# Kernel tuning notes

Measured on AMD Instinct MI355X. Metric: run time of the kernel, lower is better.

## Reference

```python
import jax, jax.numpy as jnp
import numpy as np

N = 16384          # num nodes (128 graphs x 128 turbines)
E = 262144         # edges before self loops
TURBINE_NUM = 128
D_IN = 512         # input_dim (= 2*hidden_dim1)
H1 = 256           # hidden_dim1
H2 = 256           # hidden_dim2
NEG_SLOPE = 0.2    # PyG GATConv default leaky relu slope


def _glorot(key, shape, fan_in):
    return jax.random.normal(key, shape, dtype=jnp.float32) / np.sqrt(fan_in)


def setup_inputs() -> dict:
    key = jax.random.key(0)
    ks = jax.random.split(key, 12)
    x = jax.random.normal(ks[0], (N, H2), dtype=jnp.float32)
    adj = jax.random.randint(ks[1], (2, E), 0, N, dtype=jnp.int64)
    # fc: Linear(hidden_dim2 -> hidden_dim1); stored as [in, out]
    W_fc = _glorot(ks[2], (H2, H1), H2)
    b_fc = jnp.zeros((H1,), dtype=jnp.float32)
    # gat1: GATConv(H1 -> H1, heads=2, concat)
    W1 = _glorot(ks[3], (H1, 2 * H1), H1)
    a1_src = _glorot(ks[4], (2, H1), H1)
    a1_dst = _glorot(ks[5], (2, H1), H1)
    b1 = jnp.zeros((2 * H1,), dtype=jnp.float32)
    # gat2: GATConv(D_IN -> D_IN, heads=1, concat)
    W2 = _glorot(ks[6], (D_IN, D_IN), D_IN)
    a2_src = _glorot(ks[7], (1, D_IN), D_IN)
    a2_dst = _glorot(ks[8], (1, D_IN), D_IN)
    b2 = jnp.zeros((D_IN,), dtype=jnp.float32)
    return dict(x=x, adj=adj, W_fc=W_fc, b_fc=b_fc, W1=W1, a1_src=a1_src,
                a1_dst=a1_dst, b1=b1, W2=W2, a2_src=a2_src, a2_dst=a2_dst, b2=b2)


def gat_conv(x, src, dst, W, a_src, a_dst, bias, heads, out_ch):
    """PyG GATConv (eval mode, self loops already in src/dst)."""
    n = x.shape[0]
    h = (x @ W).reshape(n, heads, out_ch)                 # [N,H,C]
    al_s = jnp.einsum('nhc,hc->nh', h, a_src)             # [N,H]
    al_d = jnp.einsum('nhc,hc->nh', h, a_dst)
    e = jax.nn.leaky_relu(al_s[src] + al_d[dst], NEG_SLOPE)  # [E,H]
    # segment softmax over incoming edges per destination node
    e_max = jax.ops.segment_max(e, dst, num_segments=n)
    e_exp = jnp.exp(e - e_max[dst])
    denom = jax.ops.segment_sum(e_exp, dst, num_segments=n)
    alpha = e_exp / (denom[dst] + 1e-16)                  # [E,H]
    msg = h[src] * alpha[:, :, None]                      # [E,H,C]
    out = jax.ops.segment_sum(msg, dst, num_segments=n)   # [N,H,C]
    return out.reshape(n, heads * out_ch) + bias


def reference(x, adj, W_fc, b_fc, W1, a1_src, a1_dst, b1, W2, a2_src, a2_dst, b2):
    # add self loops (PyG GATConv default)
    loops = jnp.arange(N, dtype=adj.dtype)
    src = jnp.concatenate([adj[0], loops])
    dst = jnp.concatenate([adj[1], loops])
    h = jax.nn.relu(x @ W_fc + b_fc)                      # fc + ReLU
    h = gat_conv(h, src, dst, W1, a1_src, a1_dst, b1, heads=2, out_ch=H1)
    h = jax.nn.relu(h)
    h = gat_conv(h, src, dst, W2, a2_src, a2_dst, b2, heads=1, out_ch=D_IN)
    y = jax.nn.relu(h)
    return y.reshape(-1, TURBINE_NUM, y.shape[1])         # [128,128,512]
```

## Files before the change

kernel.cpp:

```cpp
#include <hip/hip_runtime.h>

#define N_NODES 16384
#define N_EDGES 262144
#define E_TOT   (N_EDGES + N_NODES)
#define NEG_SLOPE 0.2f

typedef __attribute__((ext_vector_type(8))) short short8;
typedef __attribute__((ext_vector_type(4))) float floatx4;
typedef __attribute__((ext_vector_type(4))) int intx4;

__device__ __forceinline__ float bf2f(ushort u) {
    return __uint_as_float(((unsigned)u) << 16);
}
__device__ __forceinline__ ushort f2bf(float f) {
    unsigned u = __float_as_uint(f);
    u += 0x7fffu + ((u >> 16) & 1u);
    return (ushort)(u >> 16);
}
__device__ __forceinline__ float leaky(float x) {
    return x > 0.f ? x : NEG_SLOPE * x;
}

#define PREP_CAST   524288
#define PREP_T0     (PREP_CAST)
#define PREP_T1     (PREP_T0 + 65536)
#define PREP_T2     (PREP_T1 + 131072)
#define PREP_Z      (PREP_T2 + 262144)
#define PREP_ZA     (PREP_Z + 4096)
#define PREP_TOT    (PREP_ZA + 24576)

__global__ __launch_bounds__(256) void k_prep(const float* __restrict__ x,
                                              ushort* __restrict__ xb,
                                              const float* __restrict__ Wfc,
                                              ushort* __restrict__ WfcT,
                                              const float* __restrict__ W1,
                                              ushort* __restrict__ W1T,
                                              const float* __restrict__ W2,
                                              ushort* __restrict__ W2T,
                                              int* __restrict__ counts,
                                              int* __restrict__ alzero) {
    int idx = blockIdx.x * 256 + threadIdx.x;
    if (idx < PREP_CAST) {
        floatx4 v0 = *(const floatx4*)(x + (size_t)idx * 8);
        floatx4 v1 = *(const floatx4*)(x + (size_t)idx * 8 + 4);
        short8 r;
        r[0] = (short)f2bf(v0[0]); r[1] = (short)f2bf(v0[1]);
        r[2] = (short)f2bf(v0[2]); r[3] = (short)f2bf(v0[3]);
        r[4] = (short)f2bf(v1[0]); r[5] = (short)f2bf(v1[1]);
        r[6] = (short)f2bf(v1[2]); r[7] = (short)f2bf(v1[3]);
        *(short8*)(xb + (size_t)idx * 8) = r;
    } else if (idx < PREP_T1) {
        int t = idx - PREP_T0;
        int k = t >> 8, n = t & 255;
        WfcT[n * 256 + k] = f2bf(Wfc[t]);
    } else if (idx < PREP_T2) {
        int t = idx - PREP_T1;
        int k = t >> 9, n = t & 511;
        W1T[n * 256 + k] = f2bf(W1[t]);
    } else if (idx < PREP_Z) {
        int t = idx - PREP_T2;
        int k = t >> 9, n = t & 511;
        W2T[n * 512 + k] = f2bf(W2[t]);
    } else if (idx < PREP_ZA) {
        int t = idx - PREP_Z;
        *(intx4*)(counts + t * 4) = (intx4){0, 0, 0, 0};
    } else if (idx < PREP_TOT) {
        int t = idx - PREP_ZA;
        *(intx4*)(alzero + t * 4) = (intx4){0, 0, 0, 0};
    }
}

__global__ __launch_bounds__(256) void k_hist(const int* __restrict__ adj,
                                              int* __restrict__ counts) {
    int e = blockIdx.x * 256 + threadIdx.x;
    if (e < E_TOT) {
        int d = (e < N_EDGES) ? adj[N_EDGES + e] : (e - N_EDGES);
        atomicAdd(&counts[d], 1);
    }
}

__global__ __launch_bounds__(1024) void k_scan(const int* __restrict__ counts,
                                               int* __restrict__ offs,
                                               int* __restrict__ cursor) {
    __shared__ int wsum[16];
    int t = threadIdx.x, lane = t & 63, w = t >> 6;
    int local[16];
    int tot = 0;
#pragma unroll
    for (int i = 0; i < 16; i++) {
        local[i] = tot;
        tot += counts[t * 16 + i];
    }
    int incl = tot;
#pragma unroll
    for (int d = 1; d < 64; d <<= 1) {
        int v = __shfl_up(incl, d, 64);
        if (lane >= d) incl += v;
    }
    if (lane == 63) wsum[w] = incl;
    __syncthreads();
    if (w == 0) {
        int v = (lane < 16) ? wsum[lane] : 0;
#pragma unroll
        for (int d = 1; d < 16; d <<= 1) {
            int u = __shfl_up(v, d, 64);
            if (lane >= d) v += u;
        }
        if (lane < 16) wsum[lane] = v;
    }
    __syncthreads();
    int base = ((w == 0) ? 0 : wsum[w - 1]) + incl - tot;
#pragma unroll
    for (int i = 0; i < 16; i++) {
        int o = base + local[i];
        offs[t * 16 + i] = o;
        cursor[t * 16 + i] = o;
    }
    if (t == 1023) offs[N_NODES] = wsum[15];
}

__global__ __launch_bounds__(256) void k_scatter(const int* __restrict__ adj,
                                                 int* __restrict__ cursor,
                                                 int* __restrict__ esrc) {
    int e = blockIdx.x * 256 + threadIdx.x;
    if (e < E_TOT) {
        int s, d;
        if (e < N_EDGES) { s = adj[e]; d = adj[N_EDGES + e]; }
        else             { s = e - N_EDGES; d = s; }
        int pos = atomicAdd(&cursor[d], 1);
        esrc[pos] = s;
    }
}

#define GM 128
#define GN 128
#define GK 64
#define LDK2 72

__global__ __launch_bounds__(256) void gemm128(const ushort* __restrict__ A,
                                               const ushort* __restrict__ BT,
                                               const float* __restrict__ bias,
                                               ushort* __restrict__ C,
                                               int M, int Nc, int K, int relu,
                                               const float* __restrict__ asrc,
                                               const float* __restrict__ adst,
                                               float* __restrict__ als,
                                               float* __restrict__ ald,
                                               int heads) {
    __shared__ ushort As[GM * LDK2];
    __shared__ ushort Bs[GN * LDK2];
    int tid = threadIdx.x, wave = tid >> 6, lane = tid & 63;
    int quad = lane >> 4, l16 = lane & 15;
    int bm = blockIdx.x * GM, bn = blockIdx.y * GN;
    int wm = (wave & 1) * 64, wn = (wave >> 1) * 64;

    floatx4 acc[4][4];
#pragma unroll
    for (int mi = 0; mi < 4; mi++)
#pragma unroll
        for (int ni = 0; ni < 4; ni++)
            acc[mi][ni] = (floatx4){0.f, 0.f, 0.f, 0.f};

    for (int kb = 0; kb < K; kb += GK) {
        short8 av[4], bv[4];
#pragma unroll
        for (int t = 0; t < 4; t++) {
            int ci = tid + 256 * t;
            int row = ci >> 3, col = (ci & 7) * 8;
            av[t] = *(const short8*)(A + (size_t)(bm + row) * K + kb + col);
            bv[t] = *(const short8*)(BT + (size_t)(bn + row) * K + kb + col);
        }
        __syncthreads();
#pragma unroll
        for (int t = 0; t < 4; t++) {
            int ci = tid + 256 * t;
            int row = ci >> 3, col = (ci & 7) * 8;
            *(short8*)&As[row * LDK2 + col] = av[t];
            *(short8*)&Bs[row * LDK2 + col] = bv[t];
        }
        __syncthreads();

#pragma unroll
        for (int kk = 0; kk < GK; kk += 32) {
            short8 af[4], bf[4];
#pragma unroll
            for (int mi = 0; mi < 4; mi++)
                af[mi] = *(const short8*)&As[(wm + mi * 16 + l16) * LDK2 + kk + quad * 8];
#pragma unroll
            for (int ni = 0; ni < 4; ni++)
                bf[ni] = *(const short8*)&Bs[(wn + ni * 16 + l16) * LDK2 + kk + quad * 8];
#pragma unroll
            for (int mi = 0; mi < 4; mi++)
#pragma unroll
                for (int ni = 0; ni < 4; ni++)
                    acc[mi][ni] = __builtin_amdgcn_mfma_f32_16x16x32_bf16(
                        af[mi], bf[ni], acc[mi][ni], 0, 0, 0);
        }
    }

#pragma unroll
    for (int mi = 0; mi < 4; mi++) {
        int row = bm + wm + mi * 16 + quad * 4;
#pragma unroll
        for (int ni = 0; ni < 4; ni++) {
            int col = bn + wn + ni * 16 + l16;
            float bv = bias ? bias[col] : 0.f;
#pragma unroll
            for (int i = 0; i < 4; i++) {
                float v = acc[mi][ni][i] + bv;
                if (relu) v = fmaxf(v, 0.f);
                C[(size_t)(row + i) * Nc + col] = f2bf(v);
            }
        }
    }

    if (als) {
        int head = (bn + wn) >> 8;
        float aS[4], aD[4];
#pragma unroll
        for (int ni = 0; ni < 4; ni++) {
            int col = bn + wn + ni * 16 + l16;
            aS[ni] = asrc[col];
            aD[ni] = adst[col];
        }
#pragma unroll
        for (int mi = 0; mi < 4; mi++) {
#pragma unroll
            for (int i = 0; i < 4; i++) {
                float dS = 0.f, dD = 0.f;
#pragma unroll
                for (int ni = 0; ni < 4; ni++) {
                    dS += acc[mi][ni][i] * aS[ni];
                    dD += acc[mi][ni][i] * aD[ni];
                }
#pragma unroll
                for (int msk = 1; msk < 16; msk <<= 1) {
                    dS += __shfl_xor(dS, msk, 64);
                    dD += __shfl_xor(dD, msk, 64);
                }
                if (l16 == 0) {
                    int row = bm + wm + mi * 16 + quad * 4 + i;
                    atomicAdd(&als[row * heads + head], dS);
                    atomicAdd(&ald[row * heads + head], dD);
                }
            }
        }
    }
}

__global__ __launch_bounds__(256) void k_agg(const ushort* __restrict__ h,
                                             const float* __restrict__ als,
                                             const float* __restrict__ ald,
                                             const int* __restrict__ offs,
                                             const int* __restrict__ esrc,
                                             const float* __restrict__ bias,
                                             ushort* __restrict__ outb,
                                             float* __restrict__ outf,
                                             int heads) {
    int wave = threadIdx.x >> 6, lane = threadIdx.x & 63;
    int n = blockIdx.x * 4 + wave;
    int base = offs[n];
    int deg  = offs[n + 1] - base;

    int myhead = (heads == 2) ? (lane >> 5) : 0;
    int c = (heads == 2) ? (myhead * 256 + (lane & 31) * 8) : lane * 8;

    float aldh0 = ald[n * heads];
    float aldh1 = (heads == 2) ? ald[n * heads + 1] : 0.f;

    float m0 = -1e30f, m1 = -1e30f;
    for (int cb = 0; cb < deg; cb += 64) {
        int i = cb + lane;
        if (i < deg) {
            int s = esrc[base + i];
            m0 = fmaxf(m0, leaky(als[s * heads] + aldh0));
            if (heads == 2) m1 = fmaxf(m1, leaky(als[s * 2 + 1] + aldh1));
        }
    }
#pragma unroll
    for (int msk = 1; msk < 64; msk <<= 1) {
        m0 = fmaxf(m0, __shfl_xor(m0, msk, 64));
        m1 = fmaxf(m1, __shfl_xor(m1, msk, 64));
    }

    float s0 = 0.f, s1 = 0.f;
    for (int cb = 0; cb < deg; cb += 64) {
        int i = cb + lane;
        if (i < deg) {
            int s = esrc[base + i];
            s0 += __expf(leaky(als[s * heads] + aldh0) - m0);
            if (heads == 2) s1 += __expf(leaky(als[s * 2 + 1] + aldh1) - m1);
        }
    }
#pragma unroll
    for (int msk = 1; msk < 64; msk <<= 1) {
        s0 += __shfl_xor(s0, msk, 64);
        s1 += __shfl_xor(s1, msk, 64);
    }
    float inv0 = 1.f / (s0 + 1e-16f);
    float inv1 = 1.f / (s1 + 1e-16f);

    float acc[8];
#pragma unroll
    for (int q = 0; q < 8; q++) acc[q] = 0.f;
    const ushort* hc = h + c;

    for (int cb = 0; cb < deg; cb += 64) {
        int i = cb + lane;
        int sv = 0;
        float p0 = 0.f, p1 = 0.f;
        if (i < deg) {
            sv = esrc[base + i];
            p0 = __expf(leaky(als[sv * heads] + aldh0) - m0) * inv0;
            if (heads == 2) p1 = __expf(leaky(als[sv * 2 + 1] + aldh1) - m1) * inv1;
        }
        int cnt = min(64, deg - cb);
        int j = 0;
        for (; j + 4 <= cnt; j += 4) {
            int sj0 = __shfl(sv, j, 64);
            int sj1 = __shfl(sv, j + 1, 64);
            int sj2 = __shfl(sv, j + 2, 64);
            int sj3 = __shfl(sv, j + 3, 64);
            float a00 = __shfl(p0, j, 64),     a01 = __shfl(p1, j, 64);
            float a10 = __shfl(p0, j + 1, 64), a11 = __shfl(p1, j + 1, 64);
            float a20 = __shfl(p0, j + 2, 64), a21 = __shfl(p1, j + 2, 64);
            float a30 = __shfl(p0, j + 3, 64), a31 = __shfl(p1, j + 3, 64);
            float al0 = myhead ? a01 : a00;
            float al1 = myhead ? a11 : a10;
            float al2 = myhead ? a21 : a20;
            float al3 = myhead ? a31 : a30;
            short8 h0v = *(const short8*)(hc + (size_t)sj0 * 512);
            short8 h1v = *(const short8*)(hc + (size_t)sj1 * 512);
            short8 h2v = *(const short8*)(hc + (size_t)sj2 * 512);
            short8 h3v = *(const short8*)(hc + (size_t)sj3 * 512);
#pragma unroll
            for (int q = 0; q < 8; q++) {
                acc[q] += al0 * bf2f((ushort)h0v[q]);
                acc[q] += al1 * bf2f((ushort)h1v[q]);
                acc[q] += al2 * bf2f((ushort)h2v[q]);
                acc[q] += al3 * bf2f((ushort)h3v[q]);
            }
        }
        for (; j < cnt; j++) {
            int s = __shfl(sv, j, 64);
            float a0 = __shfl(p0, j, 64), a1 = __shfl(p1, j, 64);
            float al = myhead ? a1 : a0;
            short8 hv = *(const short8*)(hc + (size_t)s * 512);
#pragma unroll
            for (int q = 0; q < 8; q++) acc[q] += al * bf2f((ushort)hv[q]);
        }
    }

    float v[8];
#pragma unroll
    for (int q = 0; q < 8; q++) v[q] = fmaxf(acc[q] + bias[c + q], 0.f);
    if (outf) {
        float* op = outf + (size_t)n * 512 + c;
        *(floatx4*)op       = (floatx4){v[0], v[1], v[2], v[3]};
        *(floatx4*)(op + 4) = (floatx4){v[4], v[5], v[6], v[7]};
    } else {
        short8 r;
#pragma unroll
        for (int q = 0; q < 8; q++) r[q] = (short)f2bf(v[q]);
        *(short8*)(outb + (size_t)n * 512 + c) = r;
    }
}

extern "C" void kernel_launch(void* const* d_in, const int* in_sizes, int n_in,
                              void* d_out, int out_size, void* d_ws, size_t ws_size,
                              hipStream_t stream) {
    const float* x   = (const float*)d_in[0];
    const int*   adj = (const int*)d_in[1];
    const float* Wfc = (const float*)d_in[2];
    const float* bfc = (const float*)d_in[3];
    const float* W1  = (const float*)d_in[4];
    const float* a1s = (const float*)d_in[5];
    const float* a1d = (const float*)d_in[6];
    const float* b1  = (const float*)d_in[7];
    const float* W2  = (const float*)d_in[8];
    const float* a2s = (const float*)d_in[9];
    const float* a2d = (const float*)d_in[10];
    const float* b2  = (const float*)d_in[11];
    float* out = (float*)d_out;

    char* ws = (char*)d_ws;
    size_t off = 0;
    auto alloc = [&](size_t bytes) -> void* {
        void* p = ws + off;
        off += (bytes + 255) & ~(size_t)255;
        return p;
    };
    ushort* xb   = (ushort*)alloc((size_t)N_NODES * 256 * 2);
    ushort* h0b  = (ushort*)alloc((size_t)N_NODES * 256 * 2);
    ushort* h1b  = (ushort*)alloc((size_t)N_NODES * 512 * 2);
    ushort* g1b  = (ushort*)alloc((size_t)N_NODES * 512 * 2);
    int* counts  = (int*)alloc(N_NODES * 4);
    int* offs    = (int*)alloc((N_NODES + 1) * 4);
    int* cursor  = (int*)alloc(N_NODES * 4);
    int* esrc    = (int*)alloc(E_TOT * 4);
    ushort* WfcT = (ushort*)alloc(256 * 256 * 2);
    ushort* W1T  = (ushort*)alloc(512 * 256 * 2);
    ushort* W2T  = (ushort*)alloc(512 * 512 * 2);
    float* als1  = (float*)alloc(N_NODES * 2 * 4);
    float* ald1  = (float*)alloc(N_NODES * 2 * 4);
    float* als2  = (float*)alloc(N_NODES * 4);
    float* ald2  = (float*)alloc(N_NODES * 4);

    k_prep<<<PREP_TOT / 256, 256, 0, stream>>>(x, xb, Wfc, WfcT, W1, W1T, W2, W2T,
                                               counts, (int*)als1);

    k_hist<<<(E_TOT + 255) / 256, 256, 0, stream>>>(adj, counts);
    k_scan<<<1, 1024, 0, stream>>>(counts, offs, cursor);
    k_scatter<<<(E_TOT + 255) / 256, 256, 0, stream>>>(adj, cursor, esrc);

    gemm128<<<dim3(N_NODES / GM, 256 / GN), 256, 0, stream>>>(
        xb, WfcT, bfc, h0b, N_NODES, 256, 256, 1,
        nullptr, nullptr, nullptr, nullptr, 0);
    gemm128<<<dim3(N_NODES / GM, 512 / GN), 256, 0, stream>>>(
        h0b, W1T, nullptr, h1b, N_NODES, 512, 256, 0,
        a1s, a1d, als1, ald1, 2);
    k_agg<<<N_NODES / 4, 256, 0, stream>>>(h1b, als1, ald1, offs, esrc, b1,
                                           g1b, nullptr, 2);

    gemm128<<<dim3(N_NODES / GM, 512 / GN), 256, 0, stream>>>(
        g1b, W2T, nullptr, h1b, N_NODES, 512, 512, 0,
        a2s, a2d, als2, ald2, 1);
    k_agg<<<N_NODES / 4, 256, 0, stream>>>(h1b, als2, ald2, offs, esrc, b2,
                                           nullptr, out, 1);
}
```

Measured before the change: 262.0 us.

## Aggregate before projecting in GAT layers and fold attention vectors into weights

Uses the linearity of GAT aggregation to reorder each layer as aggregate-then-GEMM. Layer 1 now gathers 256-wide rows from the fc output instead of 512-wide projected rows, and the final GEMM writes the fp32 output directly. Attention logits come from precomputed vectors W·a, built in the prep kernel and applied in the preceding GEMM epilogue, so each layer's logits are available before its own projection. The aggregation kernel drops the two-pass max/sum softmax and instead normalises by a running exp sum in one pass. This removes the max-subtraction step, so very large logits could overflow.

```diff
diff --git a/kernel.cpp b/kernel.cpp
--- a/kernel.cpp
+++ b/kernel.cpp
@@ -22,12 +22,12 @@
 }
 
 #define PREP_CAST   524288
-#define PREP_T0     (PREP_CAST)
-#define PREP_T1     (PREP_T0 + 65536)
+#define PREP_T1     (PREP_CAST + 65536)
 #define PREP_T2     (PREP_T1 + 131072)
 #define PREP_Z      (PREP_T2 + 262144)
 #define PREP_ZA     (PREP_Z + 4096)
-#define PREP_TOT    (PREP_ZA + 24576)
+#define PREP_V      (PREP_ZA + 24576)
+#define PREP_TOT    (PREP_V + 131072)
 
 __global__ __launch_bounds__(256) void k_prep(const float* __restrict__ x,
                                               ushort* __restrict__ xb,
@@ -38,7 +38,15 @@
                                               const float* __restrict__ W2,
                                               ushort* __restrict__ W2T,
                                               int* __restrict__ counts,
-                                              int* __restrict__ alzero) {
+                                              int* __restrict__ alzero,
+                                              const float* __restrict__ a1s,
+                                              const float* __restrict__ a1d,
+                                              const float* __restrict__ a2s,
+                                              const float* __restrict__ a2d,
+                                              float* __restrict__ v1s,
+                                              float* __restrict__ v1d,
+                                              float* __restrict__ v2s,
+                                              float* __restrict__ v2d) {
     int idx = blockIdx.x * 256 + threadIdx.x;
     if (idx < PREP_CAST) {
         floatx4 v0 = *(const floatx4*)(x + (size_t)idx * 8);
@@ -50,7 +58,7 @@
         r[6] = (short)f2bf(v1[2]); r[7] = (short)f2bf(v1[3]);
         *(short8*)(xb + (size_t)idx * 8) = r;
     } else if (idx < PREP_T1) {
-        int t = idx - PREP_T0;
+        int t = idx - PREP_CAST;
         int k = t >> 8, n = t & 255;
         WfcT[n * 256 + k] = f2bf(Wfc[t]);
     } else if (idx < PREP_T2) {
@@ -64,9 +72,40 @@
     } else if (idx < PREP_ZA) {
         int t = idx - PREP_Z;
         *(intx4*)(counts + t * 4) = (intx4){0, 0, 0, 0};
-    } else if (idx < PREP_TOT) {
+    } else if (idx < PREP_V) {
         int t = idx - PREP_ZA;
         *(intx4*)(alzero + t * 4) = (intx4){0, 0, 0, 0};
+    } else if (idx < PREP_TOT) {
+        int t = idx - PREP_V;
+        int w = t >> 6, lane = t & 63;
+        int grp = w >> 9;
+        int o = w & 511;
+        float sum;
+        if (grp < 2) {
+            const float* a = grp ? a1d : a1s;
+            int h = o >> 8, k = o & 255;
+            const float* wr = W1 + (size_t)k * 512 + h * 256;
+            const float* ar = a + h * 256;
+            floatx4 wv = *(const floatx4*)(wr + lane * 4);
+            floatx4 av = *(const floatx4*)(ar + lane * 4);
+            sum = wv[0]*av[0] + wv[1]*av[1] + wv[2]*av[2] + wv[3]*av[3];
+        } else {
+            const float* a = (grp == 2) ? a2s : a2d;
+            const float* wr = W2 + (size_t)o * 512;
+            floatx4 w0 = *(const floatx4*)(wr + lane * 8);
+            floatx4 w1 = *(const floatx4*)(wr + lane * 8 + 4);
+            floatx4 a0 = *(const floatx4*)(a + lane * 8);
+            floatx4 a1 = *(const floatx4*)(a + lane * 8 + 4);
+            sum = w0[0]*a0[0] + w0[1]*a0[1] + w0[2]*a0[2] + w0[3]*a0[3]
+                + w1[0]*a1[0] + w1[1]*a1[1] + w1[2]*a1[2] + w1[3]*a1[3];
+        }
+#pragma unroll
+        for (int msk = 1; msk < 64; msk <<= 1) sum += __shfl_xor(sum, msk, 64);
+        if (lane == 0) {
+            float* dst = (grp == 0) ? v1s : (grp == 1) ? v1d
+                        : (grp == 2) ? v2s : v2d;
+            dst[o] = sum;
+        }
     }
 }
 
@@ -138,12 +177,14 @@
 #define LDK2 72
 
 __global__ __launch_bounds__(256) void gemm128(const ushort* __restrict__ A,
+                                               int lda, int agrp,
                                                const ushort* __restrict__ BT,
                                                const float* __restrict__ bias,
                                                ushort* __restrict__ C,
+                                               float* __restrict__ Cf,
                                                int M, int Nc, int K, int relu,
-                                               const float* __restrict__ asrc,
-                                               const float* __restrict__ adst,
+                                               const float* __restrict__ vs,
+                                               const float* __restrict__ vd,
                                                float* __restrict__ als,
                                                float* __restrict__ ald,
                                                int heads) {
@@ -153,6 +194,7 @@
     int quad = lane >> 4, l16 = lane & 15;
     int bm = blockIdx.x * GM, bn = blockIdx.y * GN;
     int wm = (wave & 1) * 64, wn = (wave >> 1) * 64;
+    int abase = (bn >> 8) * agrp;
 
     floatx4 acc[4][4];
 #pragma unroll
@@ -167,7 +209,7 @@
         for (int t = 0; t < 4; t++) {
             int ci = tid + 256 * t;
             int row = ci >> 3, col = (ci & 7) * 8;
-            av[t] = *(const short8*)(A + (size_t)(bm + row) * K + kb + col);
+            av[t] = *(const short8*)(A + (size_t)(bm + row) * lda + abase + kb + col);
             bv[t] = *(const short8*)(BT + (size_t)(bn + row) * K + kb + col);
         }
         __syncthreads();
@@ -209,39 +251,77 @@
             for (int i = 0; i < 4; i++) {
                 float v = acc[mi][ni][i] + bv;
                 if (relu) v = fmaxf(v, 0.f);
-                C[(size_t)(row + i) * Nc + col] = f2bf(v);
+                acc[mi][ni][i] = v;
+                if (Cf) Cf[(size_t)(row + i) * Nc + col] = v;
+                else    C[(size_t)(row + i) * Nc + col] = f2bf(v);
             }
         }
     }
 
     if (als) {
-        int head = (bn + wn) >> 8;
-        float aS[4], aD[4];
-#pragma unroll
-        for (int ni = 0; ni < 4; ni++) {
-            int col = bn + wn + ni * 16 + l16;
-            aS[ni] = asrc[col];
-            aD[ni] = adst[col];
-        }
-#pragma unroll
-        for (int mi = 0; mi < 4; mi++) {
-#pragma unroll
-            for (int i = 0; i < 4; i++) {
-                float dS = 0.f, dD = 0.f;
-#pragma unroll
-                for (int ni = 0; ni < 4; ni++) {
-                    dS += acc[mi][ni][i] * aS[ni];
-                    dD += acc[mi][ni][i] * aD[ni];
+        if (heads == 2) {
+            float s0[4], s1[4], d0[4], d1[4];
+#pragma unroll
+            for (int ni = 0; ni < 4; ni++) {
+                int col = bn + wn + ni * 16 + l16;
+                s0[ni] = vs[col];  s1[ni] = vs[256 + col];
+                d0[ni] = vd[col];  d1[ni] = vd[256 + col];
+            }
+#pragma unroll
+            for (int mi = 0; mi < 4; mi++) {
+#pragma unroll
+                for (int i = 0; i < 4; i++) {
+                    float aS0 = 0.f, aS1 = 0.f, aD0 = 0.f, aD1 = 0.f;
+#pragma unroll
+                    for (int ni = 0; ni < 4; ni++) {
+                        float vv = acc[mi][ni][i];
+                        aS0 += vv * s0[ni]; aS1 += vv * s1[ni];
+                        aD0 += vv * d0[ni]; aD1 += vv * d1[ni];
+                    }
+#pragma unroll
+                    for (int msk = 1; msk < 16; msk <<= 1) {
+                        aS0 += __shfl_xor(aS0, msk, 64);
+                        aS1 += __shfl_xor(aS1, msk, 64);
+                        aD0 += __shfl_xor(aD0, msk, 64);
+                        aD1 += __shfl_xor(aD1, msk, 64);
+                    }
+                    if (l16 == 0) {
+                        int row = bm + wm + mi * 16 + quad * 4 + i;
+                        atomicAdd(&als[row * 2],     aS0);
+                        atomicAdd(&als[row * 2 + 1], aS1);
+                        atomicAdd(&ald[row * 2],     aD0);
+                        atomicAdd(&ald[row * 2 + 1], aD1);
+                    }
                 }
-#pragma unroll
-                for (int msk = 1; msk < 16; msk <<= 1) {
-                    dS += __shfl_xor(dS, msk, 64);
-                    dD += __shfl_xor(dD, msk, 64);
-                }
-                if (l16 == 0) {
-                    int row = bm + wm + mi * 16 + quad * 4 + i;
-                    atomicAdd(&als[row * heads + head], dS);
-                    atomicAdd(&ald[row * heads + head], dD);
+            }
+        } else {
+            float aS[4], aD[4];
+#pragma unroll
+            for (int ni = 0; ni < 4; ni++) {
+                int col = bn + wn + ni * 16 + l16;
+                aS[ni] = vs[col];
+                aD[ni] = vd[col];
+            }
+#pragma unroll
+            for (int mi = 0; mi < 4; mi++) {
+#pragma unroll
+                for (int i = 0; i < 4; i++) {
+                    float dS = 0.f, dD = 0.f;
+#pragma unroll
+                    for (int ni = 0; ni < 4; ni++) {
+                        dS += acc[mi][ni][i] * aS[ni];
+                        dD += acc[mi][ni][i] * aD[ni];
+                    }
+#pragma unroll
+                    for (int msk = 1; msk < 16; msk <<= 1) {
+                        dS += __shfl_xor(dS, msk, 64);
+                        dD += __shfl_xor(dD, msk, 64);
+                    }
+                    if (l16 == 0) {
+                        int row = bm + wm + mi * 16 + quad * 4 + i;
+                        atomicAdd(&als[row], dS);
+                        atomicAdd(&ald[row], dD);
+                    }
                 }
             }
         }
@@ -253,9 +333,7 @@
                                              const float* __restrict__ ald,
                                              const int* __restrict__ offs,
                                              const int* __restrict__ esrc,
-                                             const float* __restrict__ bias,
                                              ushort* __restrict__ outb,
-                                             float* __restrict__ outf,
                                              int heads) {
     int wave = threadIdx.x >> 6, lane = threadIdx.x & 63;
     int n = blockIdx.x * 4 + wave;
@@ -263,56 +341,27 @@
     int deg  = offs[n + 1] - base;
 
     int myhead = (heads == 2) ? (lane >> 5) : 0;
-    int c = (heads == 2) ? (myhead * 256 + (lane & 31) * 8) : lane * 8;
+    int cs = (heads == 2) ? ((lane & 31) * 8) : (lane * 8);
+    int stride = (heads == 2) ? 256 : 512;
 
     float aldh0 = ald[n * heads];
     float aldh1 = (heads == 2) ? ald[n * heads + 1] : 0.f;
-
-    float m0 = -1e30f, m1 = -1e30f;
-    for (int cb = 0; cb < deg; cb += 64) {
-        int i = cb + lane;
-        if (i < deg) {
-            int s = esrc[base + i];
-            m0 = fmaxf(m0, leaky(als[s * heads] + aldh0));
-            if (heads == 2) m1 = fmaxf(m1, leaky(als[s * 2 + 1] + aldh1));
-        }
-    }
-#pragma unroll
-    for (int msk = 1; msk < 64; msk <<= 1) {
-        m0 = fmaxf(m0, __shfl_xor(m0, msk, 64));
-        m1 = fmaxf(m1, __shfl_xor(m1, msk, 64));
-    }
-
-    float s0 = 0.f, s1 = 0.f;
-    for (int cb = 0; cb < deg; cb += 64) {
-        int i = cb + lane;
-        if (i < deg) {
-            int s = esrc[base + i];
-            s0 += __expf(leaky(als[s * heads] + aldh0) - m0);
-            if (heads == 2) s1 += __expf(leaky(als[s * 2 + 1] + aldh1) - m1);
-        }
-    }
-#pragma unroll
-    for (int msk = 1; msk < 64; msk <<= 1) {
-        s0 += __shfl_xor(s0, msk, 64);
-        s1 += __shfl_xor(s1, msk, 64);
-    }
-    float inv0 = 1.f / (s0 + 1e-16f);
-    float inv1 = 1.f / (s1 + 1e-16f);
+    const ushort* hc = h + cs;
 
     float acc[8];
 #pragma unroll
     for (int q = 0; q < 8; q++) acc[q] = 0.f;
-    const ushort* hc = h + c;
+    float ws0 = 0.f, ws1 = 0.f;
 
     for (int cb = 0; cb < deg; cb += 64) {
         int i = cb + lane;
         int sv = 0;
-        float p0 = 0.f, p1 = 0.f;
+        float w0 = 0.f, w1 = 0.f;
         if (i < deg) {
             sv = esrc[base + i];
-            p0 = __expf(leaky(als[sv * heads] + aldh0) - m0) * inv0;
-            if (heads == 2) p1 = __expf(leaky(als[sv * 2 + 1] + aldh1) - m1) * inv1;
+            w0 = __expf(leaky(als[sv * heads] + aldh0));
+            if (heads == 2) w1 = __expf(leaky(als[sv * 2 + 1] + aldh1));
+            ws0 += w0; ws1 += w1;
         }
         int cnt = min(64, deg - cb);
         int j = 0;
@@ -321,18 +370,18 @@
             int sj1 = __shfl(sv, j + 1, 64);
             int sj2 = __shfl(sv, j + 2, 64);
             int sj3 = __shfl(sv, j + 3, 64);
-            float a00 = __shfl(p0, j, 64),     a01 = __shfl(p1, j, 64);
-            float a10 = __shfl(p0, j + 1, 64), a11 = __shfl(p1, j + 1, 64);
-            float a20 = __shfl(p0, j + 2, 64), a21 = __shfl(p1, j + 2, 64);
-            float a30 = __shfl(p0, j + 3, 64), a31 = __shfl(p1, j + 3, 64);
+            float a00 = __shfl(w0, j, 64),     a01 = __shfl(w1, j, 64);
+            float a10 = __shfl(w0, j + 1, 64), a11 = __shfl(w1, j + 1, 64);
+            float a20 = __shfl(w0, j + 2, 64), a21 = __shfl(w1, j + 2, 64);
+            float a30 = __shfl(w0, j + 3, 64), a31 = __shfl(w1, j + 3, 64);
             float al0 = myhead ? a01 : a00;
             float al1 = myhead ? a11 : a10;
             float al2 = myhead ? a21 : a20;
             float al3 = myhead ? a31 : a30;
-            short8 h0v = *(const short8*)(hc + (size_t)sj0 * 512);
-            short8 h1v = *(const short8*)(hc + (size_t)sj1 * 512);
-            short8 h2v = *(const short8*)(hc + (size_t)sj2 * 512);
-            short8 h3v = *(const short8*)(hc + (size_t)sj3 * 512);
+            short8 h0v = *(const short8*)(hc + (size_t)sj0 * stride);
+            short8 h1v = *(const short8*)(hc + (size_t)sj1 * stride);
+            short8 h2v = *(const short8*)(hc + (size_t)sj2 * stride);
+            short8 h3v = *(const short8*)(hc + (size_t)sj3 * stride);
 #pragma unroll
             for (int q = 0; q < 8; q++) {
                 acc[q] += al0 * bf2f((ushort)h0v[q]);
@@ -343,27 +392,25 @@
         }
         for (; j < cnt; j++) {
             int s = __shfl(sv, j, 64);
-            float a0 = __shfl(p0, j, 64), a1 = __shfl(p1, j, 64);
+            float a0 = __shfl(w0, j, 64), a1 = __shfl(w1, j, 64);
             float al = myhead ? a1 : a0;
-            short8 hv = *(const short8*)(hc + (size_t)s * 512);
+            short8 hv = *(const short8*)(hc + (size_t)s * stride);
 #pragma unroll
             for (int q = 0; q < 8; q++) acc[q] += al * bf2f((ushort)hv[q]);
         }
     }
 
-    float v[8];
-#pragma unroll
-    for (int q = 0; q < 8; q++) v[q] = fmaxf(acc[q] + bias[c + q], 0.f);
-    if (outf) {
-        float* op = outf + (size_t)n * 512 + c;
-        *(floatx4*)op       = (floatx4){v[0], v[1], v[2], v[3]};
-        *(floatx4*)(op + 4) = (floatx4){v[4], v[5], v[6], v[7]};
-    } else {
-        short8 r;
-#pragma unroll
-        for (int q = 0; q < 8; q++) r[q] = (short)f2bf(v[q]);
-        *(short8*)(outb + (size_t)n * 512 + c) = r;
-    }
+#pragma unroll
+    for (int msk = 1; msk < 64; msk <<= 1) {
+        ws0 += __shfl_xor(ws0, msk, 64);
+        ws1 += __shfl_xor(ws1, msk, 64);
+    }
+    float inv = 1.f / ((myhead ? ws1 : ws0) + 1e-16f);
+
+    short8 r;
+#pragma unroll
+    for (int q = 0; q < 8; q++) r[q] = (short)f2bf(acc[q] * inv);
+    *(short8*)(outb + (size_t)n * 512 + lane * 8) = r;
 }
 
 extern "C" void kernel_launch(void* const* d_in, const int* in_sizes, int n_in,
@@ -392,7 +439,7 @@
     };
     ushort* xb   = (ushort*)alloc((size_t)N_NODES * 256 * 2);
     ushort* h0b  = (ushort*)alloc((size_t)N_NODES * 256 * 2);
-    ushort* h1b  = (ushort*)alloc((size_t)N_NODES * 512 * 2);
+    ushort* hub  = (ushort*)alloc((size_t)N_NODES * 512 * 2);
     ushort* g1b  = (ushort*)alloc((size_t)N_NODES * 512 * 2);
     int* counts  = (int*)alloc(N_NODES * 4);
     int* offs    = (int*)alloc((N_NODES + 1) * 4);
@@ -405,26 +452,31 @@
     float* ald1  = (float*)alloc(N_NODES * 2 * 4);
     float* als2  = (float*)alloc(N_NODES * 4);
     float* ald2  = (float*)alloc(N_NODES * 4);
+    float* v1s   = (float*)alloc(512 * 4);
+    float* v1d   = (float*)alloc(512 * 4);
+    float* v2s   = (float*)alloc(512 * 4);
+    float* v2d   = (float*)alloc(512 * 4);
 
     k_prep<<<PREP_TOT / 256, 256, 0, stream>>>(x, xb, Wfc, WfcT, W1, W1T, W2, W2T,
-                                               counts, (int*)als1);
+                                               counts, (int*)als1,
+                                               a1s, a1d, a2s, a2d,
+                                               v1s, v1d, v2s, v2d);
 
     k_hist<<<(E_TOT + 255) / 256, 256, 0, stream>>>(adj, counts);
     k_scan<<<1, 1024, 0, stream>>>(counts, offs, cursor);
     k_scatter<<<(E_TOT + 255) / 256, 256, 0, stream>>>(adj, cursor, esrc);
 
     gemm128<<<dim3(N_NODES / GM, 256 / GN), 256, 0, stream>>>(
-        xb, WfcT, bfc, h0b, N_NODES, 256, 256, 1,
+        xb, 256, 0, WfcT, bfc, h0b, nullptr, N_NODES, 256, 256, 1,
+        v1s, v1d, als1, ald1, 2);
+    k_agg<<<N_NODES / 4, 256, 0, stream>>>(h0b, als1, ald1, offs, esrc, hub, 2);
+
+    gemm128<<<dim3(N_NODES / GM, 512 / GN), 256, 0, stream>>>(
+        hub, 512, 256, W1T, b1, g1b, nullptr, N_NODES, 512, 256, 1,
+        v2s, v2d, als2, ald2, 1);
+    k_agg<<<N_NODES / 4, 256, 0, stream>>>(g1b, als2, ald2, offs, esrc, hub, 1);
+
+    gemm128<<<dim3(N_NODES / GM, 512 / GN), 256, 0, stream>>>(
+        hub, 512, 0, W2T, b2, nullptr, out, N_NODES, 512, 512, 1,
         nullptr, nullptr, nullptr, nullptr, 0);
-    gemm128<<<dim3(N_NODES / GM, 512 / GN), 256, 0, stream>>>(
-        h0b, W1T, nullptr, h1b, N_NODES, 512, 256, 0,
-        a1s, a1d, als1, ald1, 2);
-    k_agg<<<N_NODES / 4, 256, 0, stream>>>(h1b, als1, ald1, offs, esrc, b1,
-                                           g1b, nullptr, 2);
-
-    gemm128<<<dim3(N_NODES / GM, 512 / GN), 256, 0, stream>>>(
-        g1b, W2T, nullptr, h1b, N_NODES, 512, 512, 0,
-        a2s, a2d, als2, ald2, 1);
-    k_agg<<<N_NODES / 4, 256, 0, stream>>>(h1b, als2, ald2, offs, esrc, b2,
-                                           nullptr, out, 1);
-}
+}
```

Measured after the change: 246.5 us. 1.06x faster.
